# Optimization experiments

Hardware: AMD Instinct MI355X
Metric: run time of the kernel (lower is better)

Reference implementation:

```python
import jax, jax.numpy as jnp
import numpy as np

B, N, NIN = 32, 128, 64
MSG_HID, MSG_OUT, N_HID, N_OUT = 256, 64, 256, 64
E = N * (N - 1)  # fully connected, no self loops


def setup_inputs() -> dict:
    key = jax.random.key(0)
    ks = jax.random.split(key, 12)

    # one-hot incidence matrices (NRI convention)
    off = np.ones((N, N), dtype=np.float32) - np.eye(N, dtype=np.float32)
    recv_idx, send_idx = np.where(off)
    eye = np.eye(N, dtype=np.float32)
    rel_rec = jnp.asarray(eye[recv_idx])    # [E, N]
    rel_send = jnp.asarray(eye[send_idx])   # [E, N]

    s = 0.05
    inp = {
        "inputs": jax.random.normal(ks[0], (B, N, NIN), jnp.float32),
        "rel_rec": rel_rec,
        "rel_send": rel_send,
        "rel_types": jax.random.uniform(ks[1], (B, E, 2), jnp.float32),
        "msg_fc1_w": jax.random.normal(ks[2], (MSG_HID, 2 * NIN), jnp.float32) * s,
        "msg_fc1_b": jnp.zeros((MSG_HID,), jnp.float32),
        "msg_fc2_w": jax.random.normal(ks[3], (MSG_OUT, MSG_HID), jnp.float32) * s,
        "msg_fc2_b": jnp.zeros((MSG_OUT,), jnp.float32),
        "out_fc1_w": jax.random.normal(ks[4], (N_HID, MSG_OUT), jnp.float32) * s,
        "out_fc1_b": jnp.zeros((N_HID,), jnp.float32),
        "out_fc2_w": jax.random.normal(ks[5], (N_HID, N_HID), jnp.float32) * s,
        "out_fc2_b": jnp.zeros((N_HID,), jnp.float32),
        "out_fc3_w": jax.random.normal(ks[6], (N_OUT, N_HID), jnp.float32) * s,
        "out_fc3_b": jnp.zeros((N_OUT,), jnp.float32),
    }
    return inp


def reference(inputs, rel_rec, rel_send, rel_types,
              msg_fc1_w, msg_fc1_b, msg_fc2_w, msg_fc2_b,
              out_fc1_w, out_fc1_b, out_fc2_w, out_fc2_b,
              out_fc3_w, out_fc3_b):
    # node2edge: gather sender / receiver node features via one-hot matmul
    senders = jnp.einsum('en,bnf->bef', rel_send, inputs)    # [B,E,NIN]
    receivers = jnp.einsum('en,bnf->bef', rel_rec, inputs)   # [B,E,NIN]
    pre_msg = jnp.concatenate([senders, receivers], axis=-1)  # [B,E,2*NIN]

    all_msgs = jnp.zeros(pre_msg.shape[:2] + (MSG_OUT,), pre_msg.dtype)
    for i in range(2):  # edge-type loop (shared weights, as in the original)
        msg = jax.nn.relu(pre_msg @ msg_fc1_w.T + msg_fc1_b)
        msg = jax.nn.relu(msg @ msg_fc2_w.T + msg_fc2_b)
        all_msgs = all_msgs + msg * rel_types[:, :, i:i + 1]

    # edge2node: scatter-add messages to receiving nodes
    agg_msgs = jnp.einsum('bem,en->bnm', all_msgs, rel_rec)   # [B,N,MSG_OUT]

    pred = jax.nn.relu(agg_msgs @ out_fc1_w.T + out_fc1_b)
    pred = jax.nn.relu(pred @ out_fc2_w.T + out_fc2_b)
    pred = pred @ out_fc3_w.T + out_fc3_b                      # [B,N,N_OUT]
    return pred
```

## Files before the change

kernel.cpp:

```cpp
#include <hip/hip_runtime.h>

#define BB 32
#define NN_ 128
#define NIN 64
#define MH 256
#define MO 64
#define NH 256
#define NO 64
#define EDGES 16256

typedef _Float16 half8 __attribute__((ext_vector_type(8)));
typedef __attribute__((ext_vector_type(4))) float f32x4;


static __device__ __forceinline__ unsigned short f2h(float f) {
    return __builtin_bit_cast(unsigned short, (_Float16)f);
}

static __device__ __forceinline__ half8 pack8h(float4 f0, float4 f1) {
    uint4 u;
    u.x = __builtin_bit_cast(unsigned, __builtin_amdgcn_cvt_pkrtz(f0.x, f0.y));
    u.y = __builtin_bit_cast(unsigned, __builtin_amdgcn_cvt_pkrtz(f0.z, f0.w));
    u.z = __builtin_bit_cast(unsigned, __builtin_amdgcn_cvt_pkrtz(f1.x, f1.y));
    u.w = __builtin_bit_cast(unsigned, __builtin_amdgcn_cvt_pkrtz(f1.z, f1.w));
    return __builtin_bit_cast(half8, u);
}

static __device__ __forceinline__ half8 addrelu(uint4 s, uint4 p) {
    half8 a = __builtin_bit_cast(half8, s) + __builtin_bit_cast(half8, p);
    half8 z = {};
    return __builtin_elementwise_max(a, z);
}

__global__ __launch_bounds__(256) void prep_kernel(
    const float* __restrict__ x, const float* __restrict__ W1,
    const float* __restrict__ b1, const float* __restrict__ W2,
    const float* __restrict__ O1, const float* __restrict__ O2,
    const float* __restrict__ O3,
    unsigned short* __restrict__ psb, unsigned short* __restrict__ prb,
    unsigned short* __restrict__ w2b, unsigned short* __restrict__ o1b,
    unsigned short* __restrict__ o2b, unsigned short* __restrict__ o3b)
{
    int blk = blockIdx.x;
    int t = threadIdx.x;
    if (blk < 256) {
        int row0 = blk << 4;
        int b = blk >> 3;
        int w = t >> 6, lane = t & 63, ml = lane & 15, q = lane >> 4;

        half8 aX[2];
        #pragma unroll
        for (int s = 0; s < 2; ++s) {
            const float* base = x + (size_t)(row0 + ml) * NIN + s * 32 + q * 8;
            aX[s] = pack8h(*(const float4*)base, *(const float4*)(base + 4));
        }

        #pragma unroll
        for (int half = 0; half < 2; ++half) {
            #pragma unroll
            for (int nt = 0; nt < 4; ++nt) {
                int col = w * 64 + nt * 16 + ml;
                const float* wrow = W1 + (size_t)col * (2 * NIN) + half * 64 + q * 8;
                f32x4 acc = (f32x4){0.f, 0.f, 0.f, 0.f};
                #pragma unroll
                for (int s = 0; s < 2; ++s) {
                    half8 bw = pack8h(*(const float4*)(wrow + 32 * s),
                                      *(const float4*)(wrow + 32 * s + 4));
                    acc = __builtin_amdgcn_mfma_f32_16x16x32_f16(aX[s], bw, acc, 0, 0, 0);
                }
                if (half == 0) {
                    #pragma unroll
                    for (int reg = 0; reg < 4; ++reg) {
                        int n = (row0 + q * 4 + reg) & 127;
                        psb[((size_t)(b * 32 + (col >> 3)) * NN_ + n) * 8 + (col & 7)]
                            = f2h(acc[reg]);
                    }
                } else {
                    float bv = b1[col];
                    #pragma unroll
                    for (int reg = 0; reg < 4; ++reg) {
                        int n = (row0 + q * 4 + reg) & 127;
                        prb[((size_t)(b * NN_) + n) * MH + col] = f2h(acc[reg] + bv);
                    }
                }
            }
        }
    } else if (blk < 320) {
        int i = ((blk - 256) << 8) + t;
        int kc4 = i >> 9, rem = i & 511;
        int n = rem >> 3, k7 = i & 7;
        w2b[i] = f2h(W2[n * MH + kc4 * 8 + k7]);
    } else {
        int i = ((blk - 320) << 8) + t;
        if (i < 16384)       o1b[i]         = f2h(O1[i]);
        else if (i < 81920)  o2b[i - 16384] = f2h(O2[i - 16384]);
        else                 o3b[i - 81920] = f2h(O3[i - 81920]);
    }
}

__global__ __launch_bounds__(512) void edge_node_kernel(
    const float* __restrict__ rt, const float* __restrict__ b2,
    const unsigned short* __restrict__ psb, const unsigned short* __restrict__ prb,
    const unsigned short* __restrict__ w2b,
    const unsigned short* __restrict__ o1b, const float* __restrict__ b1o,
    const unsigned short* __restrict__ o2b, const float* __restrict__ b2o,
    const unsigned short* __restrict__ o3b, const float* __restrict__ b3o,
    float* __restrict__ out)
{
    int blk = blockIdx.x;
    int t = threadIdx.x;
    int wv = t >> 6;
    int lane = t & 63;
    int ml = lane & 15, q = lane >> 4;

    int b = blk >> 4;
    int rbase = (blk & 15) << 3;

    __shared__ uint4 w2L[2048];
    __shared__ float rtwA[4][2][128];
    __shared__ uint4 prL[8][32];
    __shared__ float aggL[16][68];
    __shared__ __align__(16) char uni[17280];
    typedef float red_t[2][8][64];
    red_t* redA = (red_t*)uni;
    typedef unsigned short row264[264];
    row264* h1L = (row264*)uni;
    row264* h2L = (row264*)(uni + 8448);

    {
        const uint4* w24 = (const uint4*)w2b;
        #pragma unroll
        for (int i = 0; i < 4; ++i)
            w2L[t + 512 * i] = w24[t + 512 * i];
    }
    if (t < 256) {
        int r = t >> 5, c = t & 31;
        prL[r][c] = ((const uint4*)(prb + ((size_t)(b * NN_ + rbase + r)) * MH))[c];
    }
    #pragma unroll
    for (int j = 0; j < 2; ++j) {
        int idx = 2 * t + j;
        int un = idx >> 8, rr = (idx >> 7) & 1, s = idx & 127;
        int r = rbase + un * 2 + rr;
        float v = 0.f;
        if (s != r) {
            int e = r * 127 + s - (s > r ? 1 : 0);
            const float* p = rt + ((size_t)(b * EDGES + e)) * 2;
            v = p[0] + p[1];
        }
        rtwA[un][rr][s] = v;
    }

    aggL[8 + wv][lane] = 0.f;

    float b2c[4];
    #pragma unroll
    for (int nt = 0; nt < 4; ++nt) b2c[nt] = b2[16 * nt + ml];

    int slot = 16 * wv + ml;
    uint4 usr[8];
    {
        const uint4* ps4 = (const uint4*)psb + (size_t)b * (32 * NN_);
        #pragma unroll
        for (int kc = 0; kc < 8; ++kc)
            usr[kc] = ps4[(4 * kc + q) * NN_ + slot];
    }

    __syncthreads();

    #pragma unroll 1
    for (int un = 0; un < 4; ++un) {
        f32x4 acc[2][4];
        #pragma unroll
        for (int rr = 0; rr < 2; ++rr)
            #pragma unroll
            for (int nt = 0; nt < 4; ++nt)
                acc[rr][nt] = (f32x4){0.f, 0.f, 0.f, 0.f};

        #pragma unroll
        for (int kc = 0; kc < 8; ++kc) {
            int kc4 = 4 * kc + q;
            uint4 up0 = prL[un * 2][kc4];
            uint4 up1 = prL[un * 2 + 1][kc4];

            half8 a0 = addrelu(usr[kc], up0);
            half8 a1 = addrelu(usr[kc], up1);

            #pragma unroll
            for (int nt = 0; nt < 4; ++nt) {
                half8 bw = __builtin_bit_cast(half8, w2L[kc4 * 64 + 16 * nt + ml]);
                acc[0][nt] = __builtin_amdgcn_mfma_f32_16x16x32_f16(a0, bw, acc[0][nt], 0, 0, 0);
                acc[1][nt] = __builtin_amdgcn_mfma_f32_16x16x32_f16(a1, bw, acc[1][nt], 0, 0, 0);
            }
        }

        #pragma unroll
        for (int rr = 0; rr < 2; ++rr) {
            float colsum[4] = {0.f, 0.f, 0.f, 0.f};
            int srow = 16 * wv + 4 * q;
            #pragma unroll
            for (int reg = 0; reg < 4; ++reg) {
                float rw = rtwA[un][rr][srow + reg];
                #pragma unroll
                for (int nt = 0; nt < 4; ++nt)
                    colsum[nt] += fmaxf(acc[rr][nt][reg] + b2c[nt], 0.f) * rw;
            }
            #pragma unroll
            for (int nt = 0; nt < 4; ++nt) {
                colsum[nt] += __shfl_xor(colsum[nt], 16);
                colsum[nt] += __shfl_xor(colsum[nt], 32);
            }
            if (lane < 16) {
                #pragma unroll
                for (int nt = 0; nt < 4; ++nt)
                    redA[un][rr][wv][16 * nt + ml] = colsum[nt];
            }
        }
    }

    __syncthreads();
    {
        int row = t >> 6, o = t & 63;
        float s = 0.f;
        #pragma unroll
        for (int w8 = 0; w8 < 8; ++w8) s += redA[row >> 1][row & 1][w8][o];
        aggL[row][o] = s;
    }
    __syncthreads();

    half8 aA[2];
    #pragma unroll
    for (int s = 0; s < 2; ++s) {
        const float* base = &aggL[ml][32 * s + q * 8];
        aA[s] = pack8h(*(const float4*)base, *(const float4*)(base + 4));
    }

    #pragma unroll
    for (int nt = 0; nt < 2; ++nt) {
        int ntg = wv * 2 + nt;
        f32x4 acc = (f32x4){0.f, 0.f, 0.f, 0.f};
        #pragma unroll
        for (int s = 0; s < 2; ++s) {
            half8 bw = *(const half8*)(o1b + (size_t)(ntg * 16 + ml) * 64 + 32 * s + q * 8);
            acc = __builtin_amdgcn_mfma_f32_16x16x32_f16(aA[s], bw, acc, 0, 0, 0);
        }
        float bv = b1o[ntg * 16 + ml];
        #pragma unroll
        for (int reg = 0; reg < 4; ++reg)
            h1L[q * 4 + reg][ntg * 16 + ml] = f2h(fmaxf(acc[reg] + bv, 0.f));
    }
    __syncthreads();

    half8 aH[8];
    #pragma unroll
    for (int ks = 0; ks < 8; ++ks)
        aH[ks] = *(const half8*)&h1L[ml][32 * ks + q * 8];
    #pragma unroll
    for (int nt = 0; nt < 2; ++nt) {
        int ntg = wv * 2 + nt;
        const unsigned short* wrow = o2b + (size_t)(ntg * 16 + ml) * NH + q * 8;
        f32x4 acc = (f32x4){0.f, 0.f, 0.f, 0.f};
        #pragma unroll
        for (int ks = 0; ks < 8; ++ks) {
            half8 bw = *(const half8*)(wrow + 32 * ks);
            acc = __builtin_amdgcn_mfma_f32_16x16x32_f16(aH[ks], bw, acc, 0, 0, 0);
        }
        float bv = b2o[ntg * 16 + ml];
        #pragma unroll
        for (int reg = 0; reg < 4; ++reg)
            h2L[q * 4 + reg][ntg * 16 + ml] = f2h(fmaxf(acc[reg] + bv, 0.f));
    }
    __syncthreads();

    if (wv < 4) {
        #pragma unroll
        for (int ks = 0; ks < 8; ++ks)
            aH[ks] = *(const half8*)&h2L[ml][32 * ks + q * 8];
        const unsigned short* wrow = o3b + (size_t)(wv * 16 + ml) * NH + q * 8;
        f32x4 acc = (f32x4){0.f, 0.f, 0.f, 0.f};
        #pragma unroll
        for (int ks = 0; ks < 8; ++ks) {
            half8 bw = *(const half8*)(wrow + 32 * ks);
            acc = __builtin_amdgcn_mfma_f32_16x16x32_f16(aH[ks], bw, acc, 0, 0, 0);
        }
        float bv = b3o[wv * 16 + ml];
        if (q < 2) {
            #pragma unroll
            for (int reg = 0; reg < 4; ++reg)
                out[(size_t)(b * NN_ + rbase + q * 4 + reg) * NO + wv * 16 + ml]
                    = acc[reg] + bv;
        }
    }
}

extern "C" void kernel_launch(void* const* d_in, const int* in_sizes, int n_in,
                              void* d_out, int out_size, void* d_ws, size_t ws_size,
                              hipStream_t stream) {
    const float* x   = (const float*)d_in[0];
    const float* rt  = (const float*)d_in[3];
    const float* W1  = (const float*)d_in[4];
    const float* b1  = (const float*)d_in[5];
    const float* W2  = (const float*)d_in[6];
    const float* b2  = (const float*)d_in[7];
    const float* O1  = (const float*)d_in[8];
    const float* b1o = (const float*)d_in[9];
    const float* O2  = (const float*)d_in[10];
    const float* b2o = (const float*)d_in[11];
    const float* O3  = (const float*)d_in[12];
    const float* b3o = (const float*)d_in[13];

    float* ws  = (float*)d_ws;
    unsigned short* psb = (unsigned short*)ws;
    unsigned short* prb = (unsigned short*)(ws + 524288);
    unsigned short* w2b = (unsigned short*)(ws + 1048576);
    unsigned short* o1b = (unsigned short*)(ws + 1056768);
    unsigned short* o2b = (unsigned short*)(ws + 1064960);
    unsigned short* o3b = (unsigned short*)(ws + 1097728);
    float* out = (float*)d_out;

    hipLaunchKernelGGL(prep_kernel, dim3(704), dim3(256), 0, stream,
                       x, W1, b1, W2, O1, O2, O3, psb, prb, w2b, o1b, o2b, o3b);
    hipLaunchKernelGGL(edge_node_kernel, dim3(512), dim3(512), 0, stream,
                       rt, b2, psb, prb, w2b, o1b, b1o, o2b, b2o, o3b, b3o, out);
}
```

Before: 128.7 us.

## Switch edge message GEMM to 32x32x16 MFMA with 2x2 wave tiling

Replaces the 16x16x32 MFMA tiling of the second message layer (each wave owning 16 sender rows by all 64 outputs) with 32x32x16 MFMAs, where the 8 waves form a 4x2 grid of 32 rows by 32 outputs. This cuts the number of MFMA issues and LDS weight reads per wave, and the cross-wave partial reduction shrinks from 8 to 4 partials. In exchange each lane holds 16 preloaded sender vectors instead of 8, which raises register pressure, and the row-weight indexing in the epilogue becomes more involved.

```diff
diff --git a/kernel.cpp b/kernel.cpp
--- a/kernel.cpp
+++ b/kernel.cpp
@@ -11,6 +11,7 @@
 
 typedef _Float16 half8 __attribute__((ext_vector_type(8)));
 typedef __attribute__((ext_vector_type(4))) float f32x4;
+typedef __attribute__((ext_vector_type(16))) float f32x16;
 
 
 static __device__ __forceinline__ unsigned short f2h(float f) {
@@ -112,6 +113,9 @@
     int wv = t >> 6;
     int lane = t & 63;
     int ml = lane & 15, q = lane >> 4;
+    int l31 = lane & 31, h = lane >> 5;
+    int mt = wv >> 1;
+    int nt2 = wv & 1;
 
     int b = blk >> 4;
     int rbase = (blk & 15) << 3;
@@ -121,7 +125,7 @@
     __shared__ uint4 prL[8][32];
     __shared__ float aggL[16][68];
     __shared__ __align__(16) char uni[17280];
-    typedef float red_t[2][8][64];
+    typedef float red_t[2][4][64];
     red_t* redA = (red_t*)uni;
     typedef unsigned short row264[264];
     row264* h1L = (row264*)uni;
@@ -153,68 +157,48 @@
 
     aggL[8 + wv][lane] = 0.f;
 
-    float b2c[4];
-    #pragma unroll
-    for (int nt = 0; nt < 4; ++nt) b2c[nt] = b2[16 * nt + ml];
-
-    int slot = 16 * wv + ml;
-    uint4 usr[8];
+    float b2v = b2[32 * nt2 + l31];
+
+    uint4 usr[16];
     {
         const uint4* ps4 = (const uint4*)psb + (size_t)b * (32 * NN_);
         #pragma unroll
-        for (int kc = 0; kc < 8; ++kc)
-            usr[kc] = ps4[(4 * kc + q) * NN_ + slot];
+        for (int ks = 0; ks < 16; ++ks)
+            usr[ks] = ps4[(2 * ks + h) * NN_ + 32 * mt + l31];
     }
 
     __syncthreads();
 
     #pragma unroll 1
     for (int un = 0; un < 4; ++un) {
-        f32x4 acc[2][4];
-        #pragma unroll
-        for (int rr = 0; rr < 2; ++rr)
-            #pragma unroll
-            for (int nt = 0; nt < 4; ++nt)
-                acc[rr][nt] = (f32x4){0.f, 0.f, 0.f, 0.f};
-
-        #pragma unroll
-        for (int kc = 0; kc < 8; ++kc) {
-            int kc4 = 4 * kc + q;
-            uint4 up0 = prL[un * 2][kc4];
-            uint4 up1 = prL[un * 2 + 1][kc4];
-
-            half8 a0 = addrelu(usr[kc], up0);
-            half8 a1 = addrelu(usr[kc], up1);
-
-            #pragma unroll
-            for (int nt = 0; nt < 4; ++nt) {
-                half8 bw = __builtin_bit_cast(half8, w2L[kc4 * 64 + 16 * nt + ml]);
-                acc[0][nt] = __builtin_amdgcn_mfma_f32_16x16x32_f16(a0, bw, acc[0][nt], 0, 0, 0);
-                acc[1][nt] = __builtin_amdgcn_mfma_f32_16x16x32_f16(a1, bw, acc[1][nt], 0, 0, 0);
-            }
-        }
-
-        #pragma unroll
-        for (int rr = 0; rr < 2; ++rr) {
-            float colsum[4] = {0.f, 0.f, 0.f, 0.f};
-            int srow = 16 * wv + 4 * q;
-            #pragma unroll
-            for (int reg = 0; reg < 4; ++reg) {
-                float rw = rtwA[un][rr][srow + reg];
-                #pragma unroll
-                for (int nt = 0; nt < 4; ++nt)
-                    colsum[nt] += fmaxf(acc[rr][nt][reg] + b2c[nt], 0.f) * rw;
-            }
-            #pragma unroll
-            for (int nt = 0; nt < 4; ++nt) {
-                colsum[nt] += __shfl_xor(colsum[nt], 16);
-                colsum[nt] += __shfl_xor(colsum[nt], 32);
-            }
-            if (lane < 16) {
-                #pragma unroll
-                for (int nt = 0; nt < 4; ++nt)
-                    redA[un][rr][wv][16 * nt + ml] = colsum[nt];
-            }
+        f32x16 acc0 = {0.f,0.f,0.f,0.f,0.f,0.f,0.f,0.f,
+                       0.f,0.f,0.f,0.f,0.f,0.f,0.f,0.f};
+        f32x16 acc1 = acc0;
+
+        #pragma unroll
+        for (int ks = 0; ks < 16; ++ks) {
+            uint4 up0 = prL[un * 2][2 * ks + h];
+            uint4 up1 = prL[un * 2 + 1][2 * ks + h];
+            half8 a0 = addrelu(usr[ks], up0);
+            half8 a1 = addrelu(usr[ks], up1);
+            half8 bw = __builtin_bit_cast(half8,
+                           w2L[(2 * ks + h) * 64 + 32 * nt2 + l31]);
+            acc0 = __builtin_amdgcn_mfma_f32_32x32x16_f16(a0, bw, acc0, 0, 0, 0);
+            acc1 = __builtin_amdgcn_mfma_f32_32x32x16_f16(a1, bw, acc1, 0, 0, 0);
+        }
+
+        float cs0 = 0.f, cs1 = 0.f;
+        #pragma unroll
+        for (int reg = 0; reg < 16; ++reg) {
+            int row = 32 * mt + (reg & 3) + 8 * (reg >> 2) + 4 * h;
+            cs0 += fmaxf(acc0[reg] + b2v, 0.f) * rtwA[un][0][row];
+            cs1 += fmaxf(acc1[reg] + b2v, 0.f) * rtwA[un][1][row];
+        }
+        cs0 += __shfl_xor(cs0, 32);
+        cs1 += __shfl_xor(cs1, 32);
+        if (lane < 32) {
+            redA[un][0][mt][32 * nt2 + l31] = cs0;
+            redA[un][1][mt][32 * nt2 + l31] = cs1;
         }
     }
 
@@ -223,7 +207,7 @@
         int row = t >> 6, o = t & 63;
         float s = 0.f;
         #pragma unroll
-        for (int w8 = 0; w8 < 8; ++w8) s += redA[row >> 1][row & 1][w8][o];
+        for (int m4 = 0; m4 < 4; ++m4) s += redA[row >> 1][row & 1][m4][o];
         aggL[row][o] = s;
     }
     __syncthreads();
```

After: 128.1 us. About the same (-0.4%).
